# Performance work log

Measured on AMD Instinct MI355X. Metric: run time of the kernel, lower is better.

## Reference

```python
import jax, jax.numpy as jnp
import numpy as np

OFFSET_FP32 = np.uint32(1064828928)  # L-mul exponent-bias correction constant for float32


def lmul_matmul(A, B):
    """Approximate A @ B (m,n)x(n,p) via integer-add-as-multiply on float bit patterns.

    Torch ref adds bit patterns in int64 then truncates with .to(torch.uint32),
    i.e. arithmetic mod 2**32 -- identical to plain uint32 wraparound addition,
    so we stay in uint32 and avoid needing x64 mode.
    """
    Au = jax.lax.bitcast_convert_type(A, jnp.uint32)          # (m, n)
    Bu = jax.lax.bitcast_convert_type(B, jnp.uint32)          # (n, p)
    prod_bits = Au[:, :, None] + Bu[None, :, :] - OFFSET_FP32  # (m, n, p), wraps mod 2^32
    prod = jax.lax.bitcast_convert_type(prod_bits, jnp.float32)
    return prod.sum(axis=1)                                    # (m, p)


def setup_inputs() -> dict:
    key = jax.random.key(0)
    k1, k2, k3 = jax.random.split(key, 3)
    m, n, p = 256, 512, 512
    x = jax.random.normal(k1, (m, n), dtype=jnp.float32)
    bound = 1.0 / np.sqrt(n)  # kaiming_uniform(a=sqrt(5)) -> U(-1/sqrt(fan_in), 1/sqrt(fan_in))
    weight = jax.random.uniform(k2, (p, n), dtype=jnp.float32, minval=-bound, maxval=bound)
    bias = jax.random.uniform(k3, (p,), dtype=jnp.float32, minval=-bound, maxval=bound)
    return {"x": x, "weight": weight, "bias": bias}


def reference(x, weight, bias):
    out = lmul_matmul(x, weight.T)
    return out + bias
```

## Files before the change

kernel.cpp:

```cpp
#include <hip/hip_runtime.h>
#include <stdint.h>


#define OFFSET_FP32 1064828928u

constexpr int M = 256;
constexpr int N = 512;
constexpr int P = 512;

constexpr int BM = 8;
constexpr int BP = 64;
constexpr int TM = 4;

__global__ __launch_bounds__(512) void lmul_linear_kernel(
    const uint32_t* __restrict__ xb,
    const uint32_t* __restrict__ wb,
    const float*    __restrict__ bias,
    float*          __restrict__ out)
{
    __shared__ uint32_t Bs[BP][N];
    __shared__ float    Red[4][BM][BP];

    const int tid  = threadIdx.x;
    const int lane = tid & 63;
    const int wq   = __builtin_amdgcn_readfirstlane(tid >> 6);
    const int ks   = wq & 3;
    const int mq   = wq >> 2;

    const int p0 = blockIdx.y * BP;
    const int m0 = blockIdx.x * BM + mq * TM;

    auto stage_load = [&](int h, uint4* r) {
        #pragma unroll
        for (int i = 0; i < 8; ++i) {
            const int row = wq * 8 + i;
            r[i] = *(const uint4*)(wb + (size_t)(p0 + row) * N + h * 256 + lane * 4);
        }
    };
    auto stage_write = [&](int h, uint4* r) {
        #pragma unroll
        for (int i = 0; i < 8; ++i) {
            const int row = wq * 8 + i;
            uint4 v = r[i];
            v.x -= OFFSET_FP32; v.y -= OFFSET_FP32;
            v.z -= OFFSET_FP32; v.w -= OFFSET_FP32;
            *(uint4*)&Bs[row][h * 256 + ((lane ^ (row & 7)) * 4)] = v;
        }
    };

    float acc[TM][4] = {};
    const int rot = lane & 7;

    const uint32_t* xr0 = xb + (size_t)(m0 + 0) * N;
    const uint32_t* xr1 = xb + (size_t)(m0 + 1) * N;
    const uint32_t* xr2 = xb + (size_t)(m0 + 2) * N;
    const uint32_t* xr3 = xb + (size_t)(m0 + 3) * N;

    auto compute = [&](int h) {
        const uint32_t* brow = &Bs[lane][(h * 64 + ks * 16) * 4];
        const int xoff = h * 256 + ks * 64;
        #pragma unroll 8
        for (int j = 0; j < 16; ++j) {
            const uint4 b  = *(const uint4*)&brow[(j ^ rot) * 4];
            const uint4 a0 = *(const uint4*)(xr0 + xoff + j * 4);
            const uint4 a1 = *(const uint4*)(xr1 + xoff + j * 4);
            const uint4 a2 = *(const uint4*)(xr2 + xoff + j * 4);
            const uint4 a3 = *(const uint4*)(xr3 + xoff + j * 4);
            acc[0][0] += __uint_as_float(a0.x + b.x);
            acc[0][1] += __uint_as_float(a0.y + b.y);
            acc[0][2] += __uint_as_float(a0.z + b.z);
            acc[0][3] += __uint_as_float(a0.w + b.w);
            acc[1][0] += __uint_as_float(a1.x + b.x);
            acc[1][1] += __uint_as_float(a1.y + b.y);
            acc[1][2] += __uint_as_float(a1.z + b.z);
            acc[1][3] += __uint_as_float(a1.w + b.w);
            acc[2][0] += __uint_as_float(a2.x + b.x);
            acc[2][1] += __uint_as_float(a2.y + b.y);
            acc[2][2] += __uint_as_float(a2.z + b.z);
            acc[2][3] += __uint_as_float(a2.w + b.w);
            acc[3][0] += __uint_as_float(a3.x + b.x);
            acc[3][1] += __uint_as_float(a3.y + b.y);
            acc[3][2] += __uint_as_float(a3.z + b.z);
            acc[3][3] += __uint_as_float(a3.w + b.w);
        }
    };

    auto lds_barrier = [&]() {
        asm volatile("s_waitcnt lgkmcnt(0)" ::: "memory");
        __builtin_amdgcn_s_barrier();
        __builtin_amdgcn_sched_barrier(0);
    };

    uint4 w0[8], w1[8];
    stage_load(0, w0);
    stage_write(0, w0);
    stage_load(1, w1);
    lds_barrier();

    compute(0);
    stage_write(1, w1);
    lds_barrier();

    compute(1);

    #pragma unroll
    for (int r = 0; r < TM; ++r)
        Red[ks][mq * TM + r][lane] =
            (acc[r][0] + acc[r][1]) + (acc[r][2] + acc[r][3]);
    __syncthreads();

    const int rr = tid >> 6;
    const int p  = p0 + lane;
    const float s = (Red[0][rr][lane] + Red[1][rr][lane])
                  + (Red[2][rr][lane] + Red[3][rr][lane]);
    out[(size_t)(blockIdx.x * BM + rr) * P + p] = s + bias[p];
}

extern "C" void kernel_launch(void* const* d_in, const int* in_sizes, int n_in,
                              void* d_out, int out_size, void* d_ws, size_t ws_size,
                              hipStream_t stream) {
    const uint32_t* xb   = (const uint32_t*)d_in[0];
    const uint32_t* wb   = (const uint32_t*)d_in[1];
    const float*    bias = (const float*)d_in[2];
    float*          out  = (float*)d_out;

    dim3 grid(M / BM, P / BP);
    dim3 block(512);
    lmul_linear_kernel<<<grid, block, 0, stream>>>(xb, wb, bias, out);
}
```

Baseline: 64.08 us.

## Split weight staging into four K-quarters with LDS writes interleaved in compute

Replaces the two-half weight staging with four 128-wide K-quarters. Each quarter is prefetched into registers one stage ahead, and its LDS stores are interleaved into the compute loop of the previous quarter. The aim is to hide global-load and LDS-write latency behind the integer-add/float-accumulate work and to shrink register staging. It adds two extra barriers and mixes LDS stores into the inner loop, which could disturb scheduling.

Measured after the change: 63.64 us (median of 2 runs). No clear change (-0.7%).

```diff
diff --git a/kernel.cpp b/kernel.cpp
--- a/kernel.cpp
+++ b/kernel.cpp
@@ -11,6 +11,8 @@
 constexpr int BM = 8;
 constexpr int BP = 64;
 constexpr int TM = 4;
+constexpr int NQ = 4;
+constexpr int QK = 128;
 
 __global__ __launch_bounds__(512) void lmul_linear_kernel(
     const uint32_t* __restrict__ xb,
@@ -18,7 +20,7 @@
     const float*    __restrict__ bias,
     float*          __restrict__ out)
 {
-    __shared__ uint32_t Bs[BP][N];
+    __shared__ uint32_t Bs[NQ][BP][QK];
     __shared__ float    Red[4][BM][BP];
 
     const int tid  = threadIdx.x;
@@ -30,22 +32,21 @@
     const int p0 = blockIdx.y * BP;
     const int m0 = blockIdx.x * BM + mq * TM;
 
-    auto stage_load = [&](int h, uint4* r) {
+    const int g    = lane & 31;
+    const int rsel = lane >> 5;
+
+    auto qload = [&](int q, uint4* r) {
         #pragma unroll
-        for (int i = 0; i < 8; ++i) {
-            const int row = wq * 8 + i;
-            r[i] = *(const uint4*)(wb + (size_t)(p0 + row) * N + h * 256 + lane * 4);
+        for (int i = 0; i < 4; ++i) {
+            const int row = wq * 8 + i * 2 + rsel;
+            r[i] = *(const uint4*)(wb + (size_t)(p0 + row) * N + q * QK + g * 4);
         }
     };
-    auto stage_write = [&](int h, uint4* r) {
-        #pragma unroll
-        for (int i = 0; i < 8; ++i) {
-            const int row = wq * 8 + i;
-            uint4 v = r[i];
-            v.x -= OFFSET_FP32; v.y -= OFFSET_FP32;
-            v.z -= OFFSET_FP32; v.w -= OFFSET_FP32;
-            *(uint4*)&Bs[row][h * 256 + ((lane ^ (row & 7)) * 4)] = v;
-        }
+    auto qwrite1 = [&](int q, uint4 v, int i) {
+        const int row = wq * 8 + i * 2 + rsel;
+        v.x -= OFFSET_FP32; v.y -= OFFSET_FP32;
+        v.z -= OFFSET_FP32; v.w -= OFFSET_FP32;
+        *(uint4*)&Bs[q][row][(g ^ (row & 7)) * 4] = v;
     };
 
     float acc[TM][4] = {};
@@ -56,11 +57,11 @@
     const uint32_t* xr2 = xb + (size_t)(m0 + 2) * N;
     const uint32_t* xr3 = xb + (size_t)(m0 + 3) * N;
 
-    auto compute = [&](int h) {
-        const uint32_t* brow = &Bs[lane][(h * 64 + ks * 16) * 4];
-        const int xoff = h * 256 + ks * 64;
-        #pragma unroll 8
-        for (int j = 0; j < 16; ++j) {
+    auto computeq = [&](int q, bool feed, int qn, uint4* r) {
+        const uint32_t* brow = &Bs[q][lane][ks * 32];
+        const int xoff = q * QK + ks * 32;
+        #pragma unroll
+        for (int j = 0; j < 8; ++j) {
             const uint4 b  = *(const uint4*)&brow[(j ^ rot) * 4];
             const uint4 a0 = *(const uint4*)(xr0 + xoff + j * 4);
             const uint4 a1 = *(const uint4*)(xr1 + xoff + j * 4);
@@ -82,6 +83,7 @@
             acc[3][1] += __uint_as_float(a3.y + b.y);
             acc[3][2] += __uint_as_float(a3.z + b.z);
             acc[3][3] += __uint_as_float(a3.w + b.w);
+            if (feed && (j & 1)) qwrite1(qn, r[j >> 1], j >> 1);
         }
     };
 
@@ -91,17 +93,25 @@
         __builtin_amdgcn_sched_barrier(0);
     };
 
-    uint4 w0[8], w1[8];
-    stage_load(0, w0);
-    stage_write(0, w0);
-    stage_load(1, w1);
+    uint4 ra[4], rb[4];
+    qload(0, ra);
+    #pragma unroll
+    for (int i = 0; i < 4; ++i) qwrite1(0, ra[i], i);
+    qload(1, rb);
     lds_barrier();
 
-    compute(0);
-    stage_write(1, w1);
+    qload(2, ra);
+    computeq(0, true, 1, rb);
     lds_barrier();
 
-    compute(1);
+    qload(3, rb);
+    computeq(1, true, 2, ra);
+    lds_barrier();
+
+    computeq(2, true, 3, rb);
+    lds_barrier();
+
+    computeq(3, false, 0, nullptr);
 
     #pragma unroll
     for (int r = 0; r < TM; ++r)
```
